# Performance work log

Measured on AMD Instinct MI355X. Metric: run time of the kernel, lower is better.

Reference implementation:

```python
import jax, jax.numpy as jnp
import numpy as np

QUERY_DIM, FEAT_DIM, HID_DIM, OUT_DIM = 512, 2048, 512, 512
B, L, S, T = 8, 128, 100, 100


def setup_inputs() -> dict:
    key = jax.random.key(0)
    ks = jax.random.split(key, 9)
    d = {
        "query": jax.random.normal(ks[0], (B, L, QUERY_DIM), jnp.float32),
        "src": jax.random.normal(ks[1], (B, S, FEAT_DIM), jnp.float32),
        "trg": jax.random.normal(ks[2], (B, T, FEAT_DIM), jnp.float32),
        # params (LinearAct == Linear + identity act); src/trg projections share weights
        "Wq": jax.random.normal(ks[3], (QUERY_DIM, HID_DIM), jnp.float32) / np.sqrt(QUERY_DIM),
        "bq": jnp.zeros((HID_DIM,), jnp.float32),
        "Ws": jax.random.normal(ks[4], (FEAT_DIM, HID_DIM), jnp.float32) / np.sqrt(FEAT_DIM),
        "bs": jnp.zeros((HID_DIM,), jnp.float32),
        "Wo": jax.random.normal(ks[5], (HID_DIM + QUERY_DIM, OUT_DIM), jnp.float32) / np.sqrt(HID_DIM + QUERY_DIM),
        "bo": jnp.zeros((OUT_DIM,), jnp.float32),
    }
    return d


def reference(query, src, trg, Wq, bq, Ws, bs, Wo, bo):
    b, l, _ = query.shape
    s = src.shape[1]
    t = trg.shape[1]
    q = query @ Wq + bq          # b,l,k
    s_key = src @ Ws + bs        # b,s,k
    t_key = trg @ Ws + bs        # b,t,k
    hid = q.shape[-1]
    # score[b,l,s,t] = q . (s_key - t_key)/sqrt(2) / sqrt(hid) -- decomposed, no b,s,t,k tensor
    qs = jnp.einsum('blk,bsk->bls', q, s_key)
    qt = jnp.einsum('blk,btk->blt', q, t_key)
    score = (qs[:, :, :, None] - qt[:, :, None, :]) / jnp.sqrt(jnp.asarray(2.0 * hid, q.dtype))
    w = jax.nn.softmax(score.reshape(b, l, s * t), axis=-1).reshape(b, l, s, t)
    # ctx = sum_{s,t} w * (s_key - t_key)/sqrt(2), decomposed via marginals
    ws = w.sum(axis=3)           # b,l,s
    wt = w.sum(axis=2)           # b,l,t
    ctx = (jnp.einsum('bls,bsk->blk', ws, s_key) - jnp.einsum('blt,btk->blk', wt, t_key)) / jnp.sqrt(jnp.asarray(2.0, q.dtype))
    x = jnp.concatenate([query, ctx], axis=-1) @ Wo + bo
    return x
```

## Files before the change

kernel.cpp:

```cpp
#include <hip/hip_runtime.h>
#include <math.h>


typedef __attribute__((ext_vector_type(8))) short s16x8;
typedef __attribute__((ext_vector_type(4))) float f32x4;

__device__ __forceinline__ unsigned short f2bf(float f) {
    unsigned int u = __float_as_uint(f);
    return (unsigned short)((u + 0x7fffu + ((u >> 16) & 1u)) >> 16);
}

__global__ __launch_bounds__(256) void k_prep(
    const float* __restrict__ query, const float* __restrict__ src,
    const float* __restrict__ trg, const float* __restrict__ Wq,
    const float* __restrict__ Ws, const float* __restrict__ Wo,
    const float* __restrict__ bs,
    unsigned short* __restrict__ aout, unsigned short* __restrict__ abf,
    unsigned short* __restrict__ WqT, unsigned short* __restrict__ WsT,
    unsigned short* __restrict__ WoT, float* __restrict__ keys) {
    __shared__ float tile[32][33];
    const int bid = blockIdx.x, t = threadIdx.x;

    if (bid < 3712) {
        const int idx = bid * 256 + t;
        if (idx < 131072) {
            float4 v = *(const float4*)(query + (size_t)idx * 4);
            ushort4 o = make_ushort4(f2bf(v.x), f2bf(v.y), f2bf(v.z), f2bf(v.w));
            const int flat = idx * 4, m = flat >> 9, c = flat & 511;
            *(ushort4*)(aout + (size_t)m * 1024 + c) = o;
        } else if (idx < 540672) {
            const int i = idx - 131072;
            float4 v = *(const float4*)(src + (size_t)i * 4);
            *(ushort4*)(abf + (size_t)i * 4) =
                make_ushort4(f2bf(v.x), f2bf(v.y), f2bf(v.z), f2bf(v.w));
        } else {
            const int i = idx - 540672;
            float4 v = *(const float4*)(trg + (size_t)i * 4);
            *(ushort4*)(abf + 1638400 + (size_t)i * 4) =
                make_ushort4(f2bf(v.x), f2bf(v.y), f2bf(v.z), f2bf(v.w));
        }
    } else if (bid < 5504) {
        const int id = bid - 3712;
        const float* W; unsigned short* O; int K, tk, tn;
        if (id < 256)       { W = Wq; O = WqT; K = 512;  tk = id >> 4;          tn = id & 15; }
        else if (id < 1280) { W = Ws; O = WsT; K = 2048; tk = (id - 256) >> 4;  tn = (id - 256) & 15; }
        else                { W = Wo; O = WoT; K = 1024; tk = (id - 1280) >> 4; tn = (id - 1280) & 15; }
        const int row = t >> 3, c4 = (t & 7) * 4;
        float4 v = *(const float4*)(W + (size_t)(tk * 32 + row) * 512 + tn * 32 + c4);
        tile[row][c4 + 0] = v.x; tile[row][c4 + 1] = v.y;
        tile[row][c4 + 2] = v.z; tile[row][c4 + 3] = v.w;
        __syncthreads();
        ushort4 o = make_ushort4(f2bf(tile[c4 + 0][row]), f2bf(tile[c4 + 1][row]),
                                 f2bf(tile[c4 + 2][row]), f2bf(tile[c4 + 3][row]));
        *(ushort4*)(O + (size_t)(tn * 32 + row) * K + tk * 32 + c4) = o;
    } else {
        const int f = ((bid - 5504) * 256 + t) * 4;
        *(float4*)(keys + f) = *(const float4*)(bs + (f & 511));
    }
}


__device__ __forceinline__ void gemm64_atomic(
    const unsigned short* __restrict__ A, const unsigned short* __restrict__ BT,
    float* __restrict__ C, int m0, int n0, int K, int N, int kbase, int kiters,
    unsigned short* As, unsigned short* Bs) {
    const int t = threadIdx.x;
    const int lane = t & 63, wid = t >> 6;
    const int wm = (wid & 1) * 32, wn = (wid >> 1) * 32;
    const int lr = lane & 15, lq = lane >> 4;
    const int r = t >> 3, c8 = (t & 7) * 8;

    s16x8 ra0, ra1, rb0, rb1;
#define LD64(kt)                                                           \
    ra0 = *(const s16x8*)(A  + (size_t)(m0 + r)      * K + (kt) + c8);     \
    ra1 = *(const s16x8*)(A  + (size_t)(m0 + r + 32) * K + (kt) + c8);     \
    rb0 = *(const s16x8*)(BT + (size_t)(n0 + r)      * K + (kt) + c8);     \
    rb1 = *(const s16x8*)(BT + (size_t)(n0 + r + 32) * K + (kt) + c8);

    f32x4 acc[2][2] = {};
    LD64(kbase);
    for (int it = 0; it < kiters; it++) {
        __syncthreads();
        *(s16x8*)&As[r * 72 + c8]        = ra0;
        *(s16x8*)&As[(r + 32) * 72 + c8] = ra1;
        *(s16x8*)&Bs[r * 72 + c8]        = rb0;
        *(s16x8*)&Bs[(r + 32) * 72 + c8] = rb1;
        __syncthreads();
        if (it + 1 < kiters) { LD64(kbase + (it + 1) * 64); }
#pragma unroll
        for (int s = 0; s < 2; s++) {
            s16x8 a0 = *(const s16x8*)&As[(wm + lr) * 72      + s * 32 + lq * 8];
            s16x8 a1 = *(const s16x8*)&As[(wm + 16 + lr) * 72 + s * 32 + lq * 8];
            s16x8 b0 = *(const s16x8*)&Bs[(wn + lr) * 72      + s * 32 + lq * 8];
            s16x8 b1 = *(const s16x8*)&Bs[(wn + 16 + lr) * 72 + s * 32 + lq * 8];
            acc[0][0] = __builtin_amdgcn_mfma_f32_16x16x32_bf16(a0, b0, acc[0][0], 0, 0, 0);
            acc[0][1] = __builtin_amdgcn_mfma_f32_16x16x32_bf16(a0, b1, acc[0][1], 0, 0, 0);
            acc[1][0] = __builtin_amdgcn_mfma_f32_16x16x32_bf16(a1, b0, acc[1][0], 0, 0, 0);
            acc[1][1] = __builtin_amdgcn_mfma_f32_16x16x32_bf16(a1, b1, acc[1][1], 0, 0, 0);
        }
    }
#undef LD64
#pragma unroll
    for (int i = 0; i < 2; i++)
#pragma unroll
        for (int j = 0; j < 2; j++) {
            const int col = n0 + wn + j * 16 + lr;
            const int row = m0 + wm + i * 16 + lq * 4;
#pragma unroll
            for (int rr = 0; rr < 4; rr++)
                unsafeAtomicAdd(&C[(size_t)(row + rr) * N + col], acc[i][j][rr]);
        }
}

template <int MODE>
__device__ __forceinline__ void gemm32(
    const unsigned short* __restrict__ A, const unsigned short* __restrict__ BT,
    const float* __restrict__ bias, void* __restrict__ Cv,
    int m0, int n0, int KA, int KB, int N, int kbase, int kiters,
    unsigned short* As, unsigned short* Bs) {
    const int t = threadIdx.x;
    const int lane = t & 63, wid = t >> 6;
    const int wm = (wid & 1) * 16, wn = (wid >> 1) * 32;
    const int lr = lane & 15, lq = lane >> 4;
    const int r = t >> 3, c8 = (t & 7) * 8;

    s16x8 ra, rb0, rb1;
#define LD32(kt)                                                            \
    ra  = *(const s16x8*)(A  + (size_t)(m0 + r)      * KA + (kt) + c8);     \
    rb0 = *(const s16x8*)(BT + (size_t)(n0 + r)      * KB + (kt) + c8);     \
    rb1 = *(const s16x8*)(BT + (size_t)(n0 + r + 32) * KB + (kt) + c8);

    f32x4 acc[2] = {};
    LD32(kbase);
    for (int it = 0; it < kiters; it++) {
        __syncthreads();
        *(s16x8*)&As[r * 72 + c8]        = ra;
        *(s16x8*)&Bs[r * 72 + c8]        = rb0;
        *(s16x8*)&Bs[(r + 32) * 72 + c8] = rb1;
        __syncthreads();
        if (it + 1 < kiters) { LD32(kbase + (it + 1) * 64); }
#pragma unroll
        for (int s = 0; s < 2; s++) {
            s16x8 a0 = *(const s16x8*)&As[(wm + lr) * 72      + s * 32 + lq * 8];
            s16x8 b0 = *(const s16x8*)&Bs[(wn + lr) * 72      + s * 32 + lq * 8];
            s16x8 b1 = *(const s16x8*)&Bs[(wn + 16 + lr) * 72 + s * 32 + lq * 8];
            acc[0] = __builtin_amdgcn_mfma_f32_16x16x32_bf16(a0, b0, acc[0], 0, 0, 0);
            acc[1] = __builtin_amdgcn_mfma_f32_16x16x32_bf16(a0, b1, acc[1], 0, 0, 0);
        }
    }
#undef LD32
#pragma unroll
    for (int j = 0; j < 2; j++) {
        const int col = n0 + wn + j * 16 + lr;
        const int row = m0 + wm + lq * 4;
        if (MODE == 1) {
            float* C = (float*)Cv;
#pragma unroll
            for (int rr = 0; rr < 4; rr++)
                unsafeAtomicAdd(&C[(size_t)(row + rr) * N + col], acc[j][rr]);
        } else if (MODE == 0) {
            float* C = (float*)Cv;
            const float bv = bias[col];
#pragma unroll
            for (int rr = 0; rr < 4; rr++)
                C[(size_t)(row + rr) * N + col] = acc[j][rr] + bv;
        } else {
            unsigned short* C = (unsigned short*)Cv;
            const float bv = bias[col];
#pragma unroll
            for (int rr = 0; rr < 4; rr++)
                C[(size_t)(row + rr) * N + col] = f2bf(acc[j][rr] + bv);
        }
    }
}

__global__ __launch_bounds__(256) void k_stageB(
    const unsigned short* __restrict__ aoutA, const unsigned short* __restrict__ abf,
    const unsigned short* __restrict__ WqT, const unsigned short* __restrict__ WsT,
    const unsigned short* __restrict__ WoT, const float* __restrict__ bq,
    const float* __restrict__ bo, unsigned short* __restrict__ qh,
    float* __restrict__ keys, float* __restrict__ out) {
    __shared__ __align__(16) unsigned short As[64 * 72];
    __shared__ __align__(16) unsigned short Bs[64 * 72];
    const int bid = blockIdx.x;
    if (bid < 400) {
        const int c = bid / 200, rem = bid % 200;
        const int mt = rem >> 3, nt = rem & 7;
        gemm64_atomic(abf, WsT, keys, mt * 64, nt * 64, 2048, 512,
                      c * 1024, 16, As, Bs);
    } else if (bid < 656) {
        const int r = bid - 400;
        const int mt = r >> 3, nt = r & 7;
        gemm32<2>(aoutA, WqT, bq, qh, mt * 32, nt * 64, 1024, 512, 512,
                  0, 8, As, Bs);
    } else {
        const int r = bid - 656;
        const int mt = r >> 3, nt = r & 7;
        gemm32<0>(aoutA, WoT, bo, out, mt * 32, nt * 64, 1024, 1024, 512,
                  0, 8, As, Bs);
    }
}

__global__ __launch_bounds__(256) void k_scgemm(
    const unsigned short* __restrict__ qh, const float* __restrict__ keys,
    float* __restrict__ sc) {
    __shared__ __align__(16) unsigned short As[32 * 72];
    __shared__ __align__(16) unsigned short Bs[64 * 72];
    const int bid = blockIdx.x;
    const int mt = bid >> 2, nt = bid & 3;
    const int m0 = mt * 32, b = mt >> 2, n0 = nt * 64;
    const int t = threadIdx.x;
    const int lane = t & 63, wid = t >> 6;
    const int wm = (wid & 1) * 16, wn = (wid >> 1) * 32;
    const int lr = lane & 15, lq = lane >> 4;
    const int r = t >> 3, c8 = (t & 7) * 8;

    const int nA = n0 + r, nB = n0 + r + 32;
    int kr0 = (nA < 128) ? (b * 100 + nA) : (800 + b * 100 + (nA - 128));
    int kr1 = (nB < 128) ? (b * 100 + nB) : (800 + b * 100 + (nB - 128));
    kr0 = kr0 > 1599 ? 1599 : kr0;
    kr1 = kr1 > 1599 ? 1599 : kr1;

    s16x8 ra, rb0, rb1;
    auto cvt8 = [](const float* p) {
        float4 u = *(const float4*)p, w = *(const float4*)(p + 4);
        s16x8 o;
        o[0] = (short)f2bf(u.x); o[1] = (short)f2bf(u.y);
        o[2] = (short)f2bf(u.z); o[3] = (short)f2bf(u.w);
        o[4] = (short)f2bf(w.x); o[5] = (short)f2bf(w.y);
        o[6] = (short)f2bf(w.z); o[7] = (short)f2bf(w.w);
        return o;
    };
#define LDSC(kt)                                                    \
    ra  = *(const s16x8*)(qh + (size_t)(m0 + r) * 512 + (kt) + c8); \
    rb0 = cvt8(keys + (size_t)kr0 * 512 + (kt) + c8);               \
    rb1 = cvt8(keys + (size_t)kr1 * 512 + (kt) + c8);

    f32x4 acc[2] = {};
    LDSC(0);
    for (int it = 0; it < 8; it++) {
        __syncthreads();
        *(s16x8*)&As[r * 72 + c8]        = ra;
        *(s16x8*)&Bs[r * 72 + c8]        = rb0;
        *(s16x8*)&Bs[(r + 32) * 72 + c8] = rb1;
        __syncthreads();
        if (it < 7) { LDSC((it + 1) * 64); }
#pragma unroll
        for (int s = 0; s < 2; s++) {
            s16x8 a0 = *(const s16x8*)&As[(wm + lr) * 72      + s * 32 + lq * 8];
            s16x8 b0 = *(const s16x8*)&Bs[(wn + lr) * 72      + s * 32 + lq * 8];
            s16x8 b1 = *(const s16x8*)&Bs[(wn + 16 + lr) * 72 + s * 32 + lq * 8];
            acc[0] = __builtin_amdgcn_mfma_f32_16x16x32_bf16(a0, b0, acc[0], 0, 0, 0);
            acc[1] = __builtin_amdgcn_mfma_f32_16x16x32_bf16(a0, b1, acc[1], 0, 0, 0);
        }
    }
#undef LDSC
#pragma unroll
    for (int j = 0; j < 2; j++) {
        const int col = n0 + wn + j * 16 + lr;
        const int row = m0 + wm + lq * 4;
        const float scale = (col >= 128) ? -(1.0f / 32.0f) : (1.0f / 32.0f);
#pragma unroll
        for (int rr = 0; rr < 4; rr++)
            sc[(size_t)(row + rr) * 256 + col] = acc[j][rr] * scale;
    }
}

__global__ __launch_bounds__(256) void k_ctx(
    const float* __restrict__ sc, const float* __restrict__ keys,
    unsigned short* __restrict__ aout) {
    __shared__ float wbuf[200 * 33];
    __shared__ float Bs[40 * 32];

    const int t = threadIdx.x;
    const int b = blockIdx.y;
    const int n0 = blockIdx.x * 32;
    const int l0 = blockIdx.z * 32;
    const int wave = t >> 6, lane = t & 63;

    for (int i = 0; i < 8; i++) {
        const int li = wave * 8 + i;
        const float4 v = *(const float4*)(
            sc + (size_t)(b * 128 + l0 + li) * 256 + lane * 4);
        const float vv[4] = {v.x, v.y, v.z, v.w};
        const int c0 = lane * 4;
        float mS = -1e30f, mT = -1e30f;
#pragma unroll
        for (int j = 0; j < 4; j++) {
            const int col = c0 + j;
            if (col < 100) mS = fmaxf(mS, vv[j]);
            if (col >= 128 && col < 228) mT = fmaxf(mT, vv[j]);
        }
#pragma unroll
        for (int off = 32; off > 0; off >>= 1) {
            mS = fmaxf(mS, __shfl_xor(mS, off));
            mT = fmaxf(mT, __shfl_xor(mT, off));
        }
        float eS[4], eT[4], sS = 0.f, sT = 0.f;
#pragma unroll
        for (int j = 0; j < 4; j++) {
            const int col = c0 + j;
            eS[j] = (col < 100) ? __expf(vv[j] - mS) : 0.f;
            eT[j] = (col >= 128 && col < 228) ? __expf(vv[j] - mT) : 0.f;
            sS += eS[j]; sT += eT[j];
        }
#pragma unroll
        for (int off = 32; off > 0; off >>= 1) {
            sS += __shfl_xor(sS, off);
            sT += __shfl_xor(sT, off);
        }
        const float iS = 1.f / sS, iT = 1.f / sT;
#pragma unroll
        for (int j = 0; j < 4; j++) {
            const int col = c0 + j;
            if (col < 100) wbuf[col * 33 + li] = eS[j] * iS;
            if (col >= 128 && col < 228)
                wbuf[(100 + col - 128) * 33 + li] = eT[j] * iT;
        }
    }
    __syncthreads();

    const int tx = t & 7, ty = t >> 3;
    float rB[5];
    auto loadB = [&](int kbase) {
#pragma unroll
        for (int e = 0; e < 5; e++) {
            const int idx = t + e * 256;
            const int k = idx >> 5, j = idx & 31;
            const int kk = kbase + k;
            rB[e] = (kk < 100)
                ?  keys[(size_t)(b * 100 + kk) * 512 + n0 + j]
                : -keys[(size_t)(800 + b * 100 + (kk - 100)) * 512 + n0 + j];
        }
    };

    float acc[4] = {};
    loadB(0);
    for (int c5 = 0; c5 < 5; c5++) {
        __syncthreads();
#pragma unroll
        for (int e = 0; e < 5; e++) {
            const int idx = t + e * 256;
            Bs[idx] = rB[e];
        }
        __syncthreads();
        if (c5 < 4) loadB((c5 + 1) * 40);
#pragma unroll 8
        for (int k = 0; k < 40; k++) {
            const float ar = wbuf[(c5 * 40 + k) * 33 + ty];
            float br[4];
            *(float4*)br = *(const float4*)&Bs[k * 32 + tx * 4];
#pragma unroll
            for (int j = 0; j < 4; j++) acc[j] = fmaf(ar, br[j], acc[j]);
        }
    }

    const float s2 = 0.70710678118654752f;
    const int m = b * 128 + l0 + ty;
    ushort4 o = make_ushort4(f2bf(acc[0] * s2), f2bf(acc[1] * s2),
                             f2bf(acc[2] * s2), f2bf(acc[3] * s2));
    *(ushort4*)(aout + (size_t)m * 1024 + 512 + n0 + tx * 4) = o;
}

__global__ __launch_bounds__(256) void k_out(
    const unsigned short* __restrict__ aout, const unsigned short* __restrict__ WoT,
    float* __restrict__ out) {
    __shared__ __align__(16) unsigned short As[64 * 72];
    __shared__ __align__(16) unsigned short Bs[64 * 72];
    const int bid = blockIdx.x;
    const int mt = bid >> 3, nt = bid & 7;
    gemm32<1>(aout, WoT, nullptr, out, mt * 32, nt * 64, 1024, 1024, 512,
              512, 8, As, Bs);
}


extern "C" void kernel_launch(void* const* d_in, const int* in_sizes, int n_in,
                              void* d_out, int out_size, void* d_ws, size_t ws_size,
                              hipStream_t stream) {
    const float* query = (const float*)d_in[0];
    const float* src   = (const float*)d_in[1];
    const float* trg   = (const float*)d_in[2];
    const float* Wq    = (const float*)d_in[3];
    const float* bq    = (const float*)d_in[4];
    const float* Ws    = (const float*)d_in[5];
    const float* bs    = (const float*)d_in[6];
    const float* Wo    = (const float*)d_in[7];
    const float* bo    = (const float*)d_in[8];
    float* out = (float*)d_out;

    float* keys = (float*)d_ws;
    float* sc   = keys + 819200;
    unsigned short* qh  = (unsigned short*)(sc + 262144);
    unsigned short* abf = qh  + 524288;
    unsigned short* aout= abf + 3276800;
    unsigned short* wqt = aout + 1048576;
    unsigned short* wst = wqt  + 262144;
    unsigned short* wot = wst  + 1048576;

    k_prep<<<6304, 256, 0, stream>>>(query, src, trg, Wq, Ws, Wo, bs,
                                     aout, abf, wqt, wst, wot, keys);
    k_stageB<<<912, 256, 0, stream>>>(aout, abf, wqt, wst, wot, bq, bo,
                                      qh, keys, out);
    k_scgemm<<<128, 256, 0, stream>>>(qh, keys, sc);
    k_ctx<<<dim3(16, 8, 4), 256, 0, stream>>>(sc, keys, aout);
    k_out<<<256, 256, 0, stream>>>(aout, wot, out);
}
```

Baseline: 132.6 us.

## Fuse fp32-to-bf16 activation conversion into GEMM loads, drop prep staging

Activation conversion for query, src and trg moves out of the prep kernel and into the GEMM tile loaders, which now read fp32 and convert in registers. This removes the bf16 copies of the activations (and their write and re-read), and the prep kernel shrinks to the weight transposes and bias fill. The context buffer becomes a separate 512-wide array, and the final GEMM points at the bottom half of the transposed Wo. The cost is twice the global read bytes per A tile and conversion work inside the GEMM loops, which is repeated across N tiles.

```diff
diff --git a/kernel.cpp b/kernel.cpp
--- a/kernel.cpp
+++ b/kernel.cpp
@@ -10,37 +10,26 @@
     return (unsigned short)((u + 0x7fffu + ((u >> 16) & 1u)) >> 16);
 }
 
+__device__ __forceinline__ s16x8 cvt8(const float* p) {
+    float4 u = *(const float4*)p, w = *(const float4*)(p + 4);
+    s16x8 o;
+    o[0] = (short)f2bf(u.x); o[1] = (short)f2bf(u.y);
+    o[2] = (short)f2bf(u.z); o[3] = (short)f2bf(u.w);
+    o[4] = (short)f2bf(w.x); o[5] = (short)f2bf(w.y);
+    o[6] = (short)f2bf(w.z); o[7] = (short)f2bf(w.w);
+    return o;
+}
+
 __global__ __launch_bounds__(256) void k_prep(
-    const float* __restrict__ query, const float* __restrict__ src,
-    const float* __restrict__ trg, const float* __restrict__ Wq,
-    const float* __restrict__ Ws, const float* __restrict__ Wo,
-    const float* __restrict__ bs,
-    unsigned short* __restrict__ aout, unsigned short* __restrict__ abf,
+    const float* __restrict__ Wq, const float* __restrict__ Ws,
+    const float* __restrict__ Wo, const float* __restrict__ bs,
     unsigned short* __restrict__ WqT, unsigned short* __restrict__ WsT,
     unsigned short* __restrict__ WoT, float* __restrict__ keys) {
     __shared__ float tile[32][33];
     const int bid = blockIdx.x, t = threadIdx.x;
 
-    if (bid < 3712) {
-        const int idx = bid * 256 + t;
-        if (idx < 131072) {
-            float4 v = *(const float4*)(query + (size_t)idx * 4);
-            ushort4 o = make_ushort4(f2bf(v.x), f2bf(v.y), f2bf(v.z), f2bf(v.w));
-            const int flat = idx * 4, m = flat >> 9, c = flat & 511;
-            *(ushort4*)(aout + (size_t)m * 1024 + c) = o;
-        } else if (idx < 540672) {
-            const int i = idx - 131072;
-            float4 v = *(const float4*)(src + (size_t)i * 4);
-            *(ushort4*)(abf + (size_t)i * 4) =
-                make_ushort4(f2bf(v.x), f2bf(v.y), f2bf(v.z), f2bf(v.w));
-        } else {
-            const int i = idx - 540672;
-            float4 v = *(const float4*)(trg + (size_t)i * 4);
-            *(ushort4*)(abf + 1638400 + (size_t)i * 4) =
-                make_ushort4(f2bf(v.x), f2bf(v.y), f2bf(v.z), f2bf(v.w));
-        }
-    } else if (bid < 5504) {
-        const int id = bid - 3712;
+    if (bid < 1792) {
+        const int id = bid;
         const float* W; unsigned short* O; int K, tk, tn;
         if (id < 256)       { W = Wq; O = WqT; K = 512;  tk = id >> 4;          tn = id & 15; }
         else if (id < 1280) { W = Ws; O = WsT; K = 2048; tk = (id - 256) >> 4;  tn = (id - 256) & 15; }
@@ -54,39 +43,44 @@
                                  f2bf(tile[c4 + 2][row]), f2bf(tile[c4 + 3][row]));
         *(ushort4*)(O + (size_t)(tn * 32 + row) * K + tk * 32 + c4) = o;
     } else {
-        const int f = ((bid - 5504) * 256 + t) * 4;
+        const int f = ((bid - 1792) * 256 + t) * 4;
         *(float4*)(keys + f) = *(const float4*)(bs + (f & 511));
     }
 }
 
-
-__device__ __forceinline__ void gemm64_atomic(
-    const unsigned short* __restrict__ A, const unsigned short* __restrict__ BT,
-    float* __restrict__ C, int m0, int n0, int K, int N, int kbase, int kiters,
-    unsigned short* As, unsigned short* Bs) {
+__device__ __forceinline__ void gemm64_keys(
+    const float* __restrict__ src, const float* __restrict__ trg,
+    const unsigned short* __restrict__ BT, float* __restrict__ C,
+    int m0, int n0, int kbase, unsigned short* As, unsigned short* Bs) {
     const int t = threadIdx.x;
     const int lane = t & 63, wid = t >> 6;
     const int wm = (wid & 1) * 32, wn = (wid >> 1) * 32;
     const int lr = lane & 15, lq = lane >> 4;
     const int r = t >> 3, c8 = (t & 7) * 8;
 
+    const int ra_row = m0 + r, rb_row = m0 + r + 32;
+    const float* arp = (ra_row < 800) ? (src + (size_t)ra_row * 2048)
+                                      : (trg + (size_t)(ra_row - 800) * 2048);
+    const float* brp = (rb_row < 800) ? (src + (size_t)rb_row * 2048)
+                                      : (trg + (size_t)(rb_row - 800) * 2048);
+
     s16x8 ra0, ra1, rb0, rb1;
-#define LD64(kt)                                                           \
-    ra0 = *(const s16x8*)(A  + (size_t)(m0 + r)      * K + (kt) + c8);     \
-    ra1 = *(const s16x8*)(A  + (size_t)(m0 + r + 32) * K + (kt) + c8);     \
-    rb0 = *(const s16x8*)(BT + (size_t)(n0 + r)      * K + (kt) + c8);     \
-    rb1 = *(const s16x8*)(BT + (size_t)(n0 + r + 32) * K + (kt) + c8);
+#define LDK(kt)                                                            \
+    ra0 = cvt8(arp + (kt) + c8);                                           \
+    ra1 = cvt8(brp + (kt) + c8);                                           \
+    rb0 = *(const s16x8*)(BT + (size_t)(n0 + r)      * 2048 + (kt) + c8);  \
+    rb1 = *(const s16x8*)(BT + (size_t)(n0 + r + 32) * 2048 + (kt) + c8);
 
     f32x4 acc[2][2] = {};
-    LD64(kbase);
-    for (int it = 0; it < kiters; it++) {
+    LDK(kbase);
+    for (int it = 0; it < 16; it++) {
         __syncthreads();
         *(s16x8*)&As[r * 72 + c8]        = ra0;
         *(s16x8*)&As[(r + 32) * 72 + c8] = ra1;
         *(s16x8*)&Bs[r * 72 + c8]        = rb0;
         *(s16x8*)&Bs[(r + 32) * 72 + c8] = rb1;
         __syncthreads();
-        if (it + 1 < kiters) { LD64(kbase + (it + 1) * 64); }
+        if (it < 15) { LDK(kbase + (it + 1) * 64); }
 #pragma unroll
         for (int s = 0; s < 2; s++) {
             s16x8 a0 = *(const s16x8*)&As[(wm + lr) * 72      + s * 32 + lq * 8];
@@ -99,7 +93,7 @@
             acc[1][1] = __builtin_amdgcn_mfma_f32_16x16x32_bf16(a1, b1, acc[1][1], 0, 0, 0);
         }
     }
-#undef LD64
+#undef LDK
 #pragma unroll
     for (int i = 0; i < 2; i++)
 #pragma unroll
@@ -108,13 +102,13 @@
             const int row = m0 + wm + i * 16 + lq * 4;
 #pragma unroll
             for (int rr = 0; rr < 4; rr++)
-                unsafeAtomicAdd(&C[(size_t)(row + rr) * N + col], acc[i][j][rr]);
-        }
-}
-
-template <int MODE>
+                unsafeAtomicAdd(&C[(size_t)(row + rr) * 512 + col], acc[i][j][rr]);
+        }
+}
+
+template <int MODE, bool AF32>
 __device__ __forceinline__ void gemm32(
-    const unsigned short* __restrict__ A, const unsigned short* __restrict__ BT,
+    const void* __restrict__ Av, const unsigned short* __restrict__ BT,
     const float* __restrict__ bias, void* __restrict__ Cv,
     int m0, int n0, int KA, int KB, int N, int kbase, int kiters,
     unsigned short* As, unsigned short* Bs) {
@@ -123,11 +117,14 @@
     const int wm = (wid & 1) * 16, wn = (wid >> 1) * 32;
     const int lr = lane & 15, lq = lane >> 4;
     const int r = t >> 3, c8 = (t & 7) * 8;
+    const float* Af = (const float*)Av;
+    const unsigned short* Ab = (const unsigned short*)Av;
 
     s16x8 ra, rb0, rb1;
-#define LD32(kt)                                                            \
-    ra  = *(const s16x8*)(A  + (size_t)(m0 + r)      * KA + (kt) + c8);     \
-    rb0 = *(const s16x8*)(BT + (size_t)(n0 + r)      * KB + (kt) + c8);     \
+#define LD32(kt)                                                                 \
+    ra  = AF32 ? cvt8(Af + (size_t)(m0 + r) * KA + (kt) + c8)                    \
+               : *(const s16x8*)(Ab + (size_t)(m0 + r) * KA + (kt) + c8);        \
+    rb0 = *(const s16x8*)(BT + (size_t)(n0 + r)      * KB + (kt) + c8);          \
     rb1 = *(const s16x8*)(BT + (size_t)(n0 + r + 32) * KB + (kt) + c8);
 
     f32x4 acc[2] = {};
@@ -175,29 +172,29 @@
 }
 
 __global__ __launch_bounds__(256) void k_stageB(
-    const unsigned short* __restrict__ aoutA, const unsigned short* __restrict__ abf,
-    const unsigned short* __restrict__ WqT, const unsigned short* __restrict__ WsT,
-    const unsigned short* __restrict__ WoT, const float* __restrict__ bq,
-    const float* __restrict__ bo, unsigned short* __restrict__ qh,
-    float* __restrict__ keys, float* __restrict__ out) {
+    const float* __restrict__ query, const float* __restrict__ src,
+    const float* __restrict__ trg, const unsigned short* __restrict__ WqT,
+    const unsigned short* __restrict__ WsT, const unsigned short* __restrict__ WoT,
+    const float* __restrict__ bq, const float* __restrict__ bo,
+    unsigned short* __restrict__ qh, float* __restrict__ keys,
+    float* __restrict__ out) {
     __shared__ __align__(16) unsigned short As[64 * 72];
     __shared__ __align__(16) unsigned short Bs[64 * 72];
     const int bid = blockIdx.x;
     if (bid < 400) {
         const int c = bid / 200, rem = bid % 200;
         const int mt = rem >> 3, nt = rem & 7;
-        gemm64_atomic(abf, WsT, keys, mt * 64, nt * 64, 2048, 512,
-                      c * 1024, 16, As, Bs);
+        gemm64_keys(src, trg, WsT, keys, mt * 64, nt * 64, c * 1024, As, Bs);
     } else if (bid < 656) {
         const int r = bid - 400;
         const int mt = r >> 3, nt = r & 7;
-        gemm32<2>(aoutA, WqT, bq, qh, mt * 32, nt * 64, 1024, 512, 512,
-                  0, 8, As, Bs);
+        gemm32<2, true>(query, WqT, bq, qh, mt * 32, nt * 64, 512, 512, 512,
+                        0, 8, As, Bs);
     } else {
         const int r = bid - 656;
         const int mt = r >> 3, nt = r & 7;
-        gemm32<0>(aoutA, WoT, bo, out, mt * 32, nt * 64, 1024, 1024, 512,
-                  0, 8, As, Bs);
+        gemm32<0, true>(query, WoT, bo, out, mt * 32, nt * 64, 512, 1024, 512,
+                        0, 8, As, Bs);
     }
 }
 
@@ -222,15 +219,6 @@
     kr1 = kr1 > 1599 ? 1599 : kr1;
 
     s16x8 ra, rb0, rb1;
-    auto cvt8 = [](const float* p) {
-        float4 u = *(const float4*)p, w = *(const float4*)(p + 4);
-        s16x8 o;
-        o[0] = (short)f2bf(u.x); o[1] = (short)f2bf(u.y);
-        o[2] = (short)f2bf(u.z); o[3] = (short)f2bf(u.w);
-        o[4] = (short)f2bf(w.x); o[5] = (short)f2bf(w.y);
-        o[6] = (short)f2bf(w.z); o[7] = (short)f2bf(w.w);
-        return o;
-    };
 #define LDSC(kt)                                                    \
     ra  = *(const s16x8*)(qh + (size_t)(m0 + r) * 512 + (kt) + c8); \
     rb0 = cvt8(keys + (size_t)kr0 * 512 + (kt) + c8);               \
@@ -268,7 +256,7 @@
 
 __global__ __launch_bounds__(256) void k_ctx(
     const float* __restrict__ sc, const float* __restrict__ keys,
-    unsigned short* __restrict__ aout) {
+    unsigned short* __restrict__ ctxbf) {
     __shared__ float wbuf[200 * 33];
     __shared__ float Bs[40 * 32];
 
@@ -359,18 +347,19 @@
     const int m = b * 128 + l0 + ty;
     ushort4 o = make_ushort4(f2bf(acc[0] * s2), f2bf(acc[1] * s2),
                              f2bf(acc[2] * s2), f2bf(acc[3] * s2));
-    *(ushort4*)(aout + (size_t)m * 1024 + 512 + n0 + tx * 4) = o;
+    *(ushort4*)(ctxbf + (size_t)m * 512 + n0 + tx * 4) = o;
 }
 
 __global__ __launch_bounds__(256) void k_out(
-    const unsigned short* __restrict__ aout, const unsigned short* __restrict__ WoT,
+    const unsigned short* __restrict__ ctxbf,
+    const unsigned short* __restrict__ wotBot,
     float* __restrict__ out) {
     __shared__ __align__(16) unsigned short As[64 * 72];
     __shared__ __align__(16) unsigned short Bs[64 * 72];
     const int bid = blockIdx.x;
     const int mt = bid >> 3, nt = bid & 7;
-    gemm32<1>(aout, WoT, nullptr, out, mt * 32, nt * 64, 1024, 1024, 512,
-              512, 8, As, Bs);
+    gemm32<1, false>(ctxbf, wotBot, nullptr, out, mt * 32, nt * 64,
+                     512, 1024, 512, 0, 8, As, Bs);
 }
 
 
@@ -390,18 +379,16 @@
 
     float* keys = (float*)d_ws;
     float* sc   = keys + 819200;
-    unsigned short* qh  = (unsigned short*)(sc + 262144);
-    unsigned short* abf = qh  + 524288;
-    unsigned short* aout= abf + 3276800;
-    unsigned short* wqt = aout + 1048576;
-    unsigned short* wst = wqt  + 262144;
-    unsigned short* wot = wst  + 1048576;
-
-    k_prep<<<6304, 256, 0, stream>>>(query, src, trg, Wq, Ws, Wo, bs,
-                                     aout, abf, wqt, wst, wot, keys);
-    k_stageB<<<912, 256, 0, stream>>>(aout, abf, wqt, wst, wot, bq, bo,
+    unsigned short* qh    = (unsigned short*)(sc + 262144);
+    unsigned short* ctxbf = qh    + 524288;
+    unsigned short* wqt   = ctxbf + 524288;
+    unsigned short* wst   = wqt   + 262144;
+    unsigned short* wot   = wst   + 1048576;
+
+    k_prep<<<2592, 256, 0, stream>>>(Wq, Ws, Wo, bs, wqt, wst, wot, keys);
+    k_stageB<<<912, 256, 0, stream>>>(query, src, trg, wqt, wst, wot, bq, bo,
                                       qh, keys, out);
     k_scgemm<<<128, 256, 0, stream>>>(qh, keys, sc);
-    k_ctx<<<dim3(16, 8, 4), 256, 0, stream>>>(sc, keys, aout);
-    k_out<<<256, 256, 0, stream>>>(aout, wot, out);
-}
+    k_ctx<<<dim3(16, 8, 4), 256, 0, stream>>>(sc, keys, ctxbf);
+    k_out<<<256, 256, 0, stream>>>(ctxbf, wot + 512, out);
+}
```

New measurement: 134.1 us. No clear change (+1.1%).
